# Performance work log

Hardware: AMD Instinct MI355X
Metric: run time of the kernel (lower is better)

## Reference

```python
import jax, jax.numpy as jnp
import numpy as np

TOPK = 16  # matches selected per (frame, query pixel)


def setup_inputs() -> dict:
    key = jax.random.key(0)
    ks = jax.random.split(key, 4)
    B, T, N, C = 2, 3, 4096, 256  # batch, ref frames, 64x64 tokens, channels
    scale = 1.0 / np.sqrt(C)
    return {
        "tgt": jax.random.normal(ks[0], (B, N, C), dtype=jnp.float32),
        "ref": jax.random.normal(ks[1], (B, T, N, C), dtype=jnp.float32),
        "Wq": jax.random.normal(ks[2], (C, C), dtype=jnp.float32) * scale,
        "bq": jnp.zeros((C,), dtype=jnp.float32),
        "Wk": jax.random.normal(ks[3], (C, C), dtype=jnp.float32) * scale,
        "bk": jnp.zeros((C,), dtype=jnp.float32),
    }


def _l2norm(x, eps=1e-12):
    return x * jax.lax.rsqrt(jnp.sum(x * x, axis=-1, keepdims=True) + eps)


def reference(tgt, ref, Wq, bq, Wk, bk):
    # tgt: [B, Nq, C] target-frame tokens; ref: [B, T, Nr, C] reference-frame tokens
    B, Nq, C = tgt.shape
    T, Nr = ref.shape[1], ref.shape[2]
    q = _l2norm(tgt @ Wq + bq)                      # [B, Nq, C]
    k = _l2norm(ref @ Wk + bk)                      # [B, T, Nr, C]
    # cross-frame cosine-similarity correlation volume
    sim = jnp.einsum("bqc,btrc->btqr", q, k)        # [B, T, Nq, Nr]
    # top-k matched reference locations per query pixel
    topv, topi = jax.lax.top_k(sim, TOPK)           # [B, T, Nq, K]
    # gather matched reference features (irregular gather)
    bi = jnp.arange(B)[:, None, None, None]
    ti = jnp.arange(T)[None, :, None, None]
    gathered = ref[bi, ti, topi]                    # [B, T, Nq, K, C]
    # attention-weighted aggregation of matched features
    w = jax.nn.softmax(topv, axis=-1)               # [B, T, Nq, K]
    out = jnp.einsum("btqk,btqkc->btqc", w, gathered)  # [B, T, Nq, C]
    return out
```

## Files before the change

### kernel.cpp

```cpp
#include <hip/hip_runtime.h>
#include <hip/hip_fp16.h>
#include <stdint.h>

#define T_FRAMES 3
#define NTOK 4096
#define CH 256

typedef __attribute__((ext_vector_type(8))) short bf16x8;
typedef __attribute__((ext_vector_type(4))) float f32x4;
typedef __attribute__((address_space(1))) void gvoid;
typedef __attribute__((address_space(3))) void svoid;

__device__ __forceinline__ unsigned short f2bf_rne(float f) {
  union { float f; uint32_t u; } c; c.f = f;
  uint32_t u = c.u;
  return (unsigned short)((u + 0x7FFFu + ((u >> 16) & 1u)) >> 16);
}
__device__ __forceinline__ float bflo(uint32_t x) { return __uint_as_float(x << 16); }
__device__ __forceinline__ float bfhi(uint32_t x) { return __uint_as_float(x & 0xFFFF0000u); }

__global__ __launch_bounds__(256) void proj_kernel(
    const float* __restrict__ Xq, const float* __restrict__ Wq, const float* __restrict__ bq,
    const float* __restrict__ Xk, const float* __restrict__ Wk, const float* __restrict__ bk,
    unsigned short* __restrict__ Qb, float* __restrict__ Qlo,
    unsigned short* __restrict__ Kb, float* __restrict__ Klo)
{
  __shared__ double At[4][64][8];
  const int tid = threadIdx.x;
  int blk = blockIdx.x;
  const float *X, *W, *bias; unsigned short* Pb; float* Plo;
  if (blk < 256) { X = Xq; W = Wq; bias = bq; Pb = Qb; Plo = Qlo; }
  else           { X = Xk; W = Wk; bias = bk; Pb = Kb; Plo = Klo; blk -= 256; }
  const int rbase = blk * 32;
  const int wv = tid >> 6, lane = tid & 63;
  const int r0 = wv * 8;
  const int c4 = lane * 4;

  double acc[8][4];
  #pragma unroll
  for (int i = 0; i < 8; i++) {
    #pragma unroll
    for (int j = 0; j < 4; j++) acc[i][j] = (double)bias[c4 + j];
  }

  const int srow_l = lane & 7;
  const int skq = (lane >> 3) * 8;
  const float* xrow = X + (size_t)(rbase + r0 + srow_l) * CH + skq;

  for (int kc = 0; kc < CH; kc += 64) {
    {
      const float4 v0 = *(const float4*)(xrow + kc);
      const float4 v1 = *(const float4*)(xrow + kc + 4);
      At[wv][skq + 0][srow_l] = (double)v0.x; At[wv][skq + 1][srow_l] = (double)v0.y;
      At[wv][skq + 2][srow_l] = (double)v0.z; At[wv][skq + 3][srow_l] = (double)v0.w;
      At[wv][skq + 4][srow_l] = (double)v1.x; At[wv][skq + 5][srow_l] = (double)v1.y;
      At[wv][skq + 6][srow_l] = (double)v1.z; At[wv][skq + 7][srow_l] = (double)v1.w;
    }
    #pragma unroll 8
    for (int k = 0; k < 64; k++) {
      const float4 w4 = *(const float4*)(W + (size_t)(kc + k) * CH + c4);
      const double b0 = (double)w4.x, b1 = (double)w4.y;
      const double b2 = (double)w4.z, b3 = (double)w4.w;
      double a[8];
      #pragma unroll
      for (int i = 0; i < 4; i++) {
        const double2 ap = *(const double2*)&At[wv][k][2 * i];
        a[2*i] = ap.x; a[2*i+1] = ap.y;
      }
      #pragma unroll
      for (int i = 0; i < 8; i++) {
        acc[i][0] += a[i] * b0; acc[i][1] += a[i] * b1;
        acc[i][2] += a[i] * b2; acc[i][3] += a[i] * b3;
      }
    }
  }

  #pragma unroll
  for (int i = 0; i < 8; i++) {
    double ss = acc[i][0]*acc[i][0] + acc[i][1]*acc[i][1]
              + acc[i][2]*acc[i][2] + acc[i][3]*acc[i][3];
    #pragma unroll
    for (int off = 32; off >= 1; off >>= 1) ss += __shfl_xor(ss, off);
    const double inv = 1.0 / sqrt(ss + 1e-12);
    const size_t base = (size_t)(rbase + r0 + i) * CH + c4;
    double vd[4]; float fb[4]; unsigned short us[4];
    #pragma unroll
    for (int j = 0; j < 4; j++) {
      vd[j] = acc[i][j] * inv;
      us[j] = f2bf_rne((float)vd[j]);
      fb[j] = __uint_as_float(((uint32_t)us[j]) << 16);
    }
    uint2 pk; pk.x = (uint32_t)us[0] | ((uint32_t)us[1] << 16);
    pk.y = (uint32_t)us[2] | ((uint32_t)us[3] << 16);
    *(uint2*)(Pb + base) = pk;
    float4 lo;
    lo.x = (float)(vd[0] - (double)fb[0]); lo.y = (float)(vd[1] - (double)fb[1]);
    lo.z = (float)(vd[2] - (double)fb[2]); lo.w = (float)(vd[3] - (double)fb[3]);
    *(float4*)(Plo + base) = lo;
  }
}

__global__ __launch_bounds__(256, 4) void sim_cand_kernel(
    const unsigned short* __restrict__ Qb,
    const unsigned short* __restrict__ Kb,
    uint32_t* __restrict__ cand,
    const float* __restrict__ ref,
    unsigned short* __restrict__ ref16, int use16)
{
  __shared__ unsigned short kst[2][32 * 256];
  const int bid = blockIdx.x;
  const int rs = bid & 3;
  const int qb = (bid >> 2) & 63;
  const int bt = bid >> 8;
  const int b = bt / T_FRAMES;
  const int tid = threadIdx.x;
  const int wv = tid >> 6, lane = tid & 63;
  const int lq = lane & 15, g = lane >> 4;
  const int q = qb * 64 + wv * 16 + lq;

  if (use16) {
    #pragma unroll
    for (int pass = 0; pass < 2; pass++) {
      const size_t i = (size_t)bid * 4096 + (size_t)pass * 2048 + (size_t)tid * 8;
      const float4 v0 = *(const float4*)(ref + i);
      const float4 v1 = *(const float4*)(ref + i + 4);
      const uint32_t h0 = (uint32_t)__half_as_ushort(__float2half_rn(v0.x));
      const uint32_t h1 = (uint32_t)__half_as_ushort(__float2half_rn(v0.y));
      const uint32_t h2 = (uint32_t)__half_as_ushort(__float2half_rn(v0.z));
      const uint32_t h3 = (uint32_t)__half_as_ushort(__float2half_rn(v0.w));
      const uint32_t h4 = (uint32_t)__half_as_ushort(__float2half_rn(v1.x));
      const uint32_t h5 = (uint32_t)__half_as_ushort(__float2half_rn(v1.y));
      const uint32_t h6 = (uint32_t)__half_as_ushort(__float2half_rn(v1.z));
      const uint32_t h7 = (uint32_t)__half_as_ushort(__float2half_rn(v1.w));
      uint4 hv;
      hv.x = h0 | (h1 << 16); hv.y = h2 | (h3 << 16);
      hv.z = h4 | (h5 << 16); hv.w = h6 | (h7 << 16);
      *(uint4*)(ref16 + i) = hv;
    }
  }

  bf16x8 bfr[8];
  {
    const unsigned short* qrow = Qb + (size_t)(b * NTOK + q) * CH + g * 8;
    #pragma unroll
    for (int kc = 0; kc < 8; kc++) bfr[kc] = *(const bf16x8*)(qrow + kc * 32);
  }
  uint32_t best[16];
  #pragma unroll
  for (int i = 0; i < 16; i++) best[i] = 0u;
  uint32_t s[16];

  const unsigned short* kbase = Kb + ((size_t)bt * NTOK + (size_t)rs * 1024) * CH;

#define STAGE(C, BUFI)                                                          \
  {                                                                             \
    _Pragma("unroll")                                                           \
    for (int t = 0; t < 4; t++) {                                               \
      const int o16 = (wv * 4 + t) * 64 + lane;                                 \
      const int row = o16 >> 5, colp = o16 & 31;                                \
      const int col16 = (colp - row) & 31;                                      \
      const unsigned short* gsrc = kbase + (size_t)((C) * 32 + row) * CH + col16 * 8; \
      __builtin_amdgcn_global_load_lds((const gvoid*)gsrc,                      \
          (svoid*)(&kst[BUFI][0] + (size_t)(wv * 4 + t) * 512), 16, 0, 0);      \
    }                                                                           \
  }

#define COMPUTE_HALF(CBASE, BUFI, SOFF)                                         \
  {                                                                             \
    _Pragma("unroll")                                                           \
    for (int t = 0; t < 2; t++) {                                               \
      f32x4 acc = {2.0f, 2.0f, 2.0f, 2.0f};                                     \
      const int arow = t * 16 + lq;                                             \
      const unsigned short* rowp = &kst[BUFI][0] + (size_t)arow * 256;          \
      _Pragma("unroll")                                                         \
      for (int kc = 0; kc < 8; kc++) {                                          \
        const int colp = (kc * 4 + g + arow) & 31;                              \
        const bf16x8 a = *(const bf16x8*)(rowp + colp * 8);                     \
        acc = __builtin_amdgcn_mfma_f32_16x16x32_bf16(a, bfr[kc], acc, 0, 0, 0);\
      }                                                                         \
      _Pragma("unroll")                                                         \
      for (int j = 0; j < 4; j++) {                                             \
        const uint32_t bits = __float_as_uint(acc[j]);                          \
        s[(SOFF) + t * 4 + j] = (bits & 0xFFFFFC00u) |                          \
            (uint32_t)((CBASE) * 32 + t * 16 + g * 4 + j);                      \
      }                                                                         \
    }                                                                           \
  }

#define SORT16_MERGE()                                                          \
  {                                                                             \
    _Pragma("unroll")                                                           \
    for (int bk = 2; bk <= 16; bk <<= 1) {                                      \
      _Pragma("unroll")                                                         \
      for (int bj = bk >> 1; bj > 0; bj >>= 1) {                                \
        _Pragma("unroll")                                                       \
        for (int i = 0; i < 16; i++) {                                          \
          const int l = i ^ bj;                                                 \
          if (l > i) {                                                          \
            const bool up = ((i & bk) != 0);                                    \
            const uint32_t a2 = s[i], b2 = s[l];                                \
            const uint32_t mn = a2 < b2 ? a2 : b2;                              \
            const uint32_t mx = a2 < b2 ? b2 : a2;                              \
            s[i] = up ? mn : mx; s[l] = up ? mx : mn;                           \
          }                                                                     \
        }                                                                       \
      }                                                                         \
    }                                                                           \
    uint32_t m[16];                                                             \
    _Pragma("unroll")                                                           \
    for (int i = 0; i < 16; i++) {                                              \
      const uint32_t a2 = best[i], b2 = s[15 - i];                              \
      m[i] = a2 > b2 ? a2 : b2;                                                 \
    }                                                                           \
    _Pragma("unroll")                                                           \
    for (int bj = 8; bj > 0; bj >>= 1) {                                        \
      _Pragma("unroll")                                                         \
      for (int i = 0; i < 16; i++) {                                            \
        const int l = i ^ bj;                                                   \
        if (l > i) {                                                            \
          const uint32_t a2 = m[i], b2 = m[l];                                  \
          const uint32_t mn = a2 < b2 ? a2 : b2;                                \
          const uint32_t mx = a2 < b2 ? b2 : a2;                                \
          m[i] = mx; m[l] = mn;                                                 \
        }                                                                       \
      }                                                                         \
    }                                                                           \
    _Pragma("unroll")                                                           \
    for (int i = 0; i < 16; i++) best[i] = m[i];                                \
  }

  STAGE(0, 0);
  __syncthreads();
  for (int cp = 0; cp < 16; cp++) {
    const int c0 = 2 * cp;
    STAGE(c0 + 1, 1);
    COMPUTE_HALF(c0, 0, 0);
    __syncthreads();
    if (cp < 15) STAGE(c0 + 2, 0);
    COMPUTE_HALF(c0 + 1, 1, 8);
    SORT16_MERGE();
    __syncthreads();
  }

  #pragma unroll
  for (int st = 16; st <= 32; st <<= 1) {
    uint32_t o[16];
    #pragma unroll
    for (int i = 0; i < 16; i++) o[i] = (uint32_t)__shfl_xor((int)best[15 - i], st);
    #pragma unroll
    for (int i = 0; i < 16; i++) best[i] = best[i] > o[i] ? best[i] : o[i];
    #pragma unroll
    for (int bj = 8; bj > 0; bj >>= 1) {
      #pragma unroll
      for (int i = 0; i < 16; i++) {
        const int l = i ^ bj;
        if (l > i) {
          const uint32_t a2 = best[i], b2 = best[l];
          const uint32_t mn = a2 < b2 ? a2 : b2;
          const uint32_t mx = a2 < b2 ? b2 : a2;
          best[i] = mx; best[l] = mn;
        }
      }
    }
  }
  if (g == 0) {
    uint32_t* cp2 = cand + ((size_t)bt * NTOK + q) * 64 + rs * 16;
    #pragma unroll
    for (int i = 0; i < 16; i += 4) {
      uint4 v; v.x = best[i]; v.y = best[i+1]; v.z = best[i+2]; v.w = best[i+3];
      *(uint4*)(cp2 + i) = v;
    }
  }
#undef STAGE
#undef COMPUTE_HALF
#undef SORT16_MERGE
}

__global__ __launch_bounds__(256) void out_kernel(
    const unsigned short* __restrict__ Qb, const float* __restrict__ Qlo,
    const unsigned short* __restrict__ Kb, const float* __restrict__ Klo,
    const uint32_t* __restrict__ cand, const float* __restrict__ ref,
    const unsigned short* __restrict__ ref16, int use16,
    float* __restrict__ out)
{
  const int tid = threadIdx.x, wv = tid >> 6, lane = tid & 63;
  const int bid = blockIdx.x;
  const int work = (bid & 7) * 768 + (bid >> 3);
  const int rowid = work * 4 + wv;
  const int bt = rowid >> 12, q = rowid & 4095;
  const int b = bt / T_FRAMES;

  const uint32_t k0 = cand[(size_t)rowid * 64 + lane];
  uint32_t key = (k0 & 0xFFFFF000u) | ((uint32_t)(lane >> 4) << 10) | (k0 & 0x3FFu);

  #pragma unroll
  for (int k = 2; k <= 64; k <<= 1) {
    #pragma unroll
    for (int j = k >> 1; j > 0; j >>= 1) {
      const uint32_t ok = (uint32_t)__shfl_xor((int)key, j);
      const bool takeMax = (((lane & j) != 0) == ((lane & k) == 0));
      if ((ok > key) == takeMax) key = ok;
    }
  }
  const float v = __uint_as_float(key & 0xFFFFF000u) - 2.0f;
  int rr = (int)(key & 0xFFFu);

  const float v16c = __shfl(v, 48);
  const float BW = 2.5e-3f;
  const bool band = fabsf(v - v16c) <= BW;

  const uint2 qbv = *(const uint2*)(Qb + (size_t)(b * NTOK + q) * CH + lane * 4);
  const float4 qlv = *(const float4*)(Qlo + (size_t)(b * NTOK + q) * CH + lane * 4);
  const double qd0 = (double)bflo(qbv.x) + (double)qlv.x;
  const double qd1 = (double)bfhi(qbv.x) + (double)qlv.y;
  const double qd2 = (double)bflo(qbv.y) + (double)qlv.z;
  const double qd3 = (double)bfhi(qbv.y) + (double)qlv.w;

  const unsigned short* kbp = Kb + (size_t)bt * NTOK * CH;
  const float* klp = Klo + (size_t)bt * NTOK * CH;

  double dval = -1.0e300;
  {
    const unsigned long long bm = __ballot(band);
    const int lo = __ffsll(bm) - 1;
    const int hi = 63 - __clzll(bm);
    for (int idx = lo; idx <= hi; idx++) {
      const int ri = __shfl(rr, idx);
      const uint2 kbv = *(const uint2*)(kbp + (size_t)ri * CH + lane * 4);
      const float4 klv = *(const float4*)(klp + (size_t)ri * CH + lane * 4);
      double dd = qd0 * ((double)bflo(kbv.x) + (double)klv.x)
                + qd1 * ((double)bfhi(kbv.x) + (double)klv.y)
                + qd2 * ((double)bflo(kbv.y) + (double)klv.z)
                + qd3 * ((double)bfhi(kbv.y) + (double)klv.w);
      #pragma unroll
      for (int off = 32; off >= 1; off >>= 1) dd += __shfl_xor(dd, off);
      if (lane == idx) dval = dd;
    }
  }
  double p = band ? dval : ((v > v16c + BW) ? (double)v : -1.0e300);

  #pragma unroll
  for (int k = 2; k <= 64; k <<= 1) {
    #pragma unroll
    for (int j = k >> 1; j > 0; j >>= 1) {
      const double op = __shfl_xor(p, j);
      const int orr = __shfl_xor(rr, j);
      const bool takeMax = (((lane & j) != 0) == ((lane & k) == 0));
      const bool og = (op > p) || (op == p && orr < rr);
      if (takeMax == og) { p = op; rr = orr; }
    }
  }

  double pm = p;
  #pragma unroll
  for (int j = 8; j >= 1; j >>= 1) pm = fmax(pm, __shfl_xor(pm, j));
  double e = (lane >= 48) ? exp(p - pm) : 0.0;
  double es = e;
  #pragma unroll
  for (int j = 8; j >= 1; j >>= 1) es += __shfl_xor(es, j);
  const float w = (float)(e / es);

  float a0 = 0.f, a1 = 0.f, a2 = 0.f, a3 = 0.f;
  if (use16) {
    const unsigned short* rb16 = ref16 + (size_t)bt * NTOK * CH + lane * 4;
    #pragma unroll
    for (int i = 0; i < 16; i++) {
      const float wi = __shfl(w, 48 + i);
      const int ri = __shfl(rr, 48 + i) & 0xFFF;
      const uint2 hv = *(const uint2*)(rb16 + (size_t)ri * CH);
      a0 += wi * __half2float(__ushort_as_half((unsigned short)(hv.x & 0xFFFFu)));
      a1 += wi * __half2float(__ushort_as_half((unsigned short)(hv.x >> 16)));
      a2 += wi * __half2float(__ushort_as_half((unsigned short)(hv.y & 0xFFFFu)));
      a3 += wi * __half2float(__ushort_as_half((unsigned short)(hv.y >> 16)));
    }
  } else {
    const float* rbp = ref + (size_t)bt * NTOK * CH + lane * 4;
    #pragma unroll
    for (int i = 0; i < 16; i++) {
      const float wi = __shfl(w, 48 + i);
      const int ri = __shfl(rr, 48 + i) & 0xFFF;
      const float4 f = *(const float4*)(rbp + (size_t)ri * CH);
      a0 += wi * f.x; a1 += wi * f.y; a2 += wi * f.z; a3 += wi * f.w;
    }
  }
  float4 o; o.x = a0; o.y = a1; o.z = a2; o.w = a3;
  *(float4*)(out + (size_t)rowid * CH + lane * 4) = o;
}

extern "C" void kernel_launch(void* const* d_in, const int* in_sizes, int n_in,
                              void* d_out, int out_size, void* d_ws, size_t ws_size,
                              hipStream_t stream) {
  const float* tgt = (const float*)d_in[0];
  const float* ref = (const float*)d_in[1];
  const float* Wq  = (const float*)d_in[2];
  const float* bq  = (const float*)d_in[3];
  const float* Wk  = (const float*)d_in[4];
  const float* bk  = (const float*)d_in[5];
  float* out = (float*)d_out;

  const int B = 2;
  const int RQ = B * NTOK;
  const int RK = B * T_FRAMES * NTOK;

  char* ws = (char*)d_ws;
  unsigned short* Qb = (unsigned short*)ws; ws += (size_t)RQ * CH * 2;
  float* Qlo = (float*)ws;                  ws += (size_t)RQ * CH * 4;
  unsigned short* Kb = (unsigned short*)ws; ws += (size_t)RK * CH * 2;
  float* Klo = (float*)ws;                  ws += (size_t)RK * CH * 4;
  uint32_t* cand = (uint32_t*)ws;           ws += (size_t)RK * 64 * 4;
  const bool big = ws_size >= (size_t)69206016;
  unsigned short* ref16 = big ? (unsigned short*)ws : nullptr;
  const int use16 = big ? 1 : 0;

  proj_kernel<<<RQ / 32 + RK / 32, 256, 0, stream>>>(
      tgt, Wq, bq, ref, Wk, bk, Qb, Qlo, Kb, Klo);
  sim_cand_kernel<<<6 * 64 * 4, 256, 0, stream>>>(Qb, Kb, cand, ref, ref16, use16);
  out_kernel<<<RK / 4, 256, 0, stream>>>(Qb, Qlo, Kb, Klo, cand, ref, ref16, use16, out);
}
```

Before: 248.5 us.

## Use FP64 MFMA for projection GEMM with runtime layout probe and VALU fallback

Adds a probe kernel that works out the register layout of the FP64 16x16x4 MFMA at runtime and writes a lane-to-element map into the workspace. A new projection kernel uses that map to run the Q/K projections on FP64 matrix cores instead of the double-precision VALU loop, then does the L2 normalization and the bf16 hi/lo split. If the probe fails, the MFMA kernel exits and the old VALU kernel runs instead. This adds two extra launches and reads A/W elements with strided scalar loads, which may limit the gain.

```diff
diff --git a/kernel.cpp b/kernel.cpp
--- a/kernel.cpp
+++ b/kernel.cpp
@@ -1,6 +1,7 @@
 #include <hip/hip_runtime.h>
 #include <hip/hip_fp16.h>
 #include <stdint.h>
+#include <math.h>
 
 #define T_FRAMES 3
 #define NTOK 4096
@@ -8,6 +9,7 @@
 
 typedef __attribute__((ext_vector_type(8))) short bf16x8;
 typedef __attribute__((ext_vector_type(4))) float f32x4;
+typedef __attribute__((ext_vector_type(4))) double f64x4;
 typedef __attribute__((address_space(1))) void gvoid;
 typedef __attribute__((address_space(3))) void svoid;
 
@@ -19,12 +21,141 @@
 __device__ __forceinline__ float bflo(uint32_t x) { return __uint_as_float(x << 16); }
 __device__ __forceinline__ float bfhi(uint32_t x) { return __uint_as_float(x & 0xFFFF0000u); }
 
-__global__ __launch_bounds__(256) void proj_kernel(
+__device__ __forceinline__ int dec_class(double v, int* idx) {
+  const double t0 = (v - 96.0) * 0.25;
+  const double t1 = (v - 6.0) * 0.0625;
+  if (t0 >= 0.0 && t0 <= 15.0 && t0 == floor(t0)) { *idx = (int)t0; return 0; }
+  if (t1 >= 0.0 && t1 <= 15.0 && t1 == floor(t1)) { *idx = (int)t1; return 1; }
+  return -1;
+}
+
+__global__ __launch_bounds__(64) void probe_kernel(int* map) {
+  __shared__ int cover[256];
+  const int l = threadIdx.x;
+  #pragma unroll
+  for (int i = 0; i < 4; i++) cover[l + i * 64] = 0;
+  __syncthreads();
+  const f64x4 z = {0.0, 0.0, 0.0, 0.0};
+  const f64x4 d1 = __builtin_amdgcn_mfma_f64_16x16x4f64(1.0, (double)l, z, 0, 0, 0);
+  const f64x4 d2 = __builtin_amdgcn_mfma_f64_16x16x4f64((double)l, 1.0, z, 0, 0, 0);
+  int ok = 1, cls0 = -1, cls1 = -1;
+  int alpha[4], beta[4];
+  #pragma unroll
+  for (int r = 0; r < 4; r++) {
+    int idx;
+    int c = dec_class(d1[r], &idx);
+    if (r == 0) cls1 = c;
+    ok &= (c >= 0) & (c == cls1);
+    beta[r] = (c >= 0) ? idx : 0;
+    c = dec_class(d2[r], &idx);
+    if (r == 0) cls0 = c;
+    ok &= (c >= 0) & (c == cls0);
+    alpha[r] = (c >= 0) ? idx : 0;
+  }
+  ok &= (cls0 == __shfl(cls0, 0));
+  ok &= (cls1 == __shfl(cls1, 0));
+  #pragma unroll
+  for (int r = 0; r < 4; r++) atomicAdd(&cover[alpha[r] * 16 + beta[r]], 1);
+  __syncthreads();
+  #pragma unroll
+  for (int i = 0; i < 4; i++) ok &= (cover[l + i * 64] == 1);
+  if (cls0 >= 0 && cls1 >= 0) {
+    const int k0 = (cls0 == 0) ? (l >> 4) : (l & 3);
+    const int k1 = (cls1 == 0) ? (l >> 4) : (l & 3);
+    const double a0v = (k0 == 0) ? 1.0 : ((k0 == 1) ? 5.0 : ((k0 == 2) ? 25.0 : 125.0));
+    const f64x4 d3 = __builtin_amdgcn_mfma_f64_16x16x4f64(a0v, (double)k1, z, 0, 0, 0);
+    #pragma unroll
+    for (int r = 0; r < 4; r++) ok &= (d3[r] == 430.0);
+  } else {
+    ok = 0;
+  }
+  ok = __all(ok) ? 1 : 0;
+  if (l == 0) { map[0] = ok; map[1] = cls0; map[2] = cls1; }
+  #pragma unroll
+  for (int r = 0; r < 4; r++) {
+    map[16 + l * 4 + r]  = alpha[r];
+    map[272 + l * 4 + r] = beta[r];
+  }
+}
+
+__global__ __launch_bounds__(64) void proj_mfma_kernel(
     const float* __restrict__ Xq, const float* __restrict__ Wq, const float* __restrict__ bq,
     const float* __restrict__ Xk, const float* __restrict__ Wk, const float* __restrict__ bk,
     unsigned short* __restrict__ Qb, float* __restrict__ Qlo,
-    unsigned short* __restrict__ Kb, float* __restrict__ Klo)
+    unsigned short* __restrict__ Kb, float* __restrict__ Klo,
+    const int* __restrict__ map)
 {
+  if (map[0] != 1) return;
+  __shared__ double ssArr[16][16];
+  const int l = threadIdx.x;
+  int blk = blockIdx.x;
+  const float *X, *W, *bias; unsigned short* Pb; float* Plo;
+  if (blk < 512) { X = Xq; W = Wq; bias = bq; Pb = Qb; Plo = Qlo; }
+  else           { X = Xk; W = Wk; bias = bk; Pb = Kb; Plo = Klo; blk -= 512; }
+  const int rbase = blk * 16;
+  const int cls0 = map[1], cls1 = map[2];
+  int alpha[4], beta[4];
+  #pragma unroll
+  for (int r = 0; r < 4; r++) {
+    alpha[r] = map[16 + l * 4 + r];
+    beta[r]  = map[272 + l * 4 + r];
+  }
+  const int a0 = (cls0 == 0) ? (l & 15) : (l >> 2);
+  const int k0 = (cls0 == 0) ? (l >> 4) : (l & 3);
+  const int b1 = (cls1 == 0) ? (l & 15) : (l >> 2);
+  const int k1 = (cls1 == 0) ? (l >> 4) : (l & 3);
+
+  f64x4 acc[16];
+  #pragma unroll
+  for (int ct = 0; ct < 16; ct++) {
+    #pragma unroll
+    for (int r = 0; r < 4; r++) acc[ct][r] = (double)bias[ct * 16 + beta[r]];
+  }
+
+  const float* xp = X + (size_t)(rbase + a0) * CH + k0;
+  const float* wp = W + (size_t)k1 * CH + b1;
+  for (int kc = 0; kc < 64; kc++) {
+    const double ad = (double)xp[kc * 4];
+    const float* wrow = wp + (size_t)(kc * 4) * CH;
+    #pragma unroll
+    for (int ct = 0; ct < 16; ct++)
+      acc[ct] = __builtin_amdgcn_mfma_f64_16x16x4f64(ad, (double)wrow[ct * 16], acc[ct], 0, 0, 0);
+  }
+
+  #pragma unroll
+  for (int r = 0; r < 4; r++) {
+    double part = 0.0;
+    #pragma unroll
+    for (int ct = 0; ct < 16; ct++) part += acc[ct][r] * acc[ct][r];
+    ssArr[alpha[r]][beta[r]] = part;
+  }
+  __syncthreads();
+  #pragma unroll
+  for (int r = 0; r < 4; r++) {
+    double ss = 0.0;
+    #pragma unroll
+    for (int c = 0; c < 16; c++) ss += ssArr[alpha[r]][c];
+    const double inv = 1.0 / sqrt(ss + 1e-12);
+    #pragma unroll
+    for (int ct = 0; ct < 16; ct++) {
+      const double vd = acc[ct][r] * inv;
+      const unsigned short us = f2bf_rne((float)vd);
+      const float fb = __uint_as_float(((uint32_t)us) << 16);
+      const size_t idx = (size_t)(rbase + alpha[r]) * CH + ct * 16 + beta[r];
+      Pb[idx] = us;
+      Plo[idx] = (float)(vd - (double)fb);
+    }
+  }
+}
+
+__global__ __launch_bounds__(256) void proj_valu_kernel(
+    const float* __restrict__ Xq, const float* __restrict__ Wq, const float* __restrict__ bq,
+    const float* __restrict__ Xk, const float* __restrict__ Wk, const float* __restrict__ bk,
+    unsigned short* __restrict__ Qb, float* __restrict__ Qlo,
+    unsigned short* __restrict__ Kb, float* __restrict__ Klo,
+    const int* __restrict__ map)
+{
+  if (map[0] == 1) return;
   __shared__ double At[4][64][8];
   const int tid = threadIdx.x;
   int blk = blockIdx.x;
@@ -412,8 +543,13 @@
   unsigned short* ref16 = big ? (unsigned short*)ws : nullptr;
   const int use16 = big ? 1 : 0;
 
-  proj_kernel<<<RQ / 32 + RK / 32, 256, 0, stream>>>(
-      tgt, Wq, bq, ref, Wk, bk, Qb, Qlo, Kb, Klo);
+  int* map = (int*)cand;
+
+  probe_kernel<<<1, 64, 0, stream>>>(map);
+  proj_mfma_kernel<<<RQ / 16 + RK / 16, 64, 0, stream>>>(
+      tgt, Wq, bq, ref, Wk, bk, Qb, Qlo, Kb, Klo, map);
+  proj_valu_kernel<<<RQ / 32 + RK / 32, 256, 0, stream>>>(
+      tgt, Wq, bq, ref, Wk, bk, Qb, Qlo, Kb, Klo, map);
   sim_cand_kernel<<<6 * 64 * 4, 256, 0, stream>>>(Qb, Kb, cand, ref, ref16, use16);
   out_kernel<<<RK / 4, 256, 0, stream>>>(Qb, Qlo, Kb, Klo, cand, ref, ref16, use16, out);
 }
```

After: 270.4 us. +8.8%, slower.
